# Performance work log

Measured on AMD Instinct MI355X. Metric: run time of the kernel, lower is better.

Reference implementation:

```python
import jax, jax.numpy as jnp
import numpy as np

EMBED_DIM = 1024
NUM_HEADS = 16
HEAD_DIM = EMBED_DIM // NUM_HEADS
SCALE = float(np.sqrt(HEAD_DIM))


def setup_inputs() -> dict:
    key = jax.random.key(0)
    ks = jax.random.split(key, 5)
    B, S, D = 4, 2048, EMBED_DIM
    lim_qkv = 1.0 / np.sqrt(D)
    lim_out = 1.0 / np.sqrt(D)
    return {
        "x": jax.random.normal(ks[0], (B, S, D), dtype=jnp.float32),
        "qkv_w": jax.random.uniform(ks[1], (3 * D, D), jnp.float32, -lim_qkv, lim_qkv),
        "qkv_b": jax.random.uniform(ks[2], (3 * D,), jnp.float32, -lim_qkv, lim_qkv),
        "out_w": jax.random.uniform(ks[3], (D, D), jnp.float32, -lim_out, lim_out),
        "out_b": jax.random.uniform(ks[4], (D,), jnp.float32, -lim_out, lim_out),
    }


def reference(x, qkv_w, qkv_b, out_w, out_b):
    B, S, D = x.shape
    H, Hd = NUM_HEADS, HEAD_DIM
    # qkv projection (torch Linear: x @ W.T + b)
    qkv = x @ qkv_w.T + qkv_b                      # [B, S, 3D]
    qkv = qkv.reshape(B, S, 3, H, Hd)
    q = jnp.transpose(qkv[:, :, 0], (0, 2, 1, 3))  # [B, H, S, Hd]
    k = jnp.transpose(qkv[:, :, 1], (0, 2, 1, 3))
    v = jnp.transpose(qkv[:, :, 2], (0, 2, 1, 3))
    attn = jnp.einsum("bhqd,bhkd->bhqk", q, k) / SCALE  # [B, H, S, S]
    attn = jax.nn.softmax(attn, axis=-1)
    out = jnp.einsum("bhqk,bhkd->bhqd", attn, v)        # [B, H, S, Hd]
    out = jnp.transpose(out, (0, 2, 1, 3)).reshape(B, S, D)
    return out @ out_w.T + out_b
```

## Files before the change

kernel.cpp:

```cpp
#include <hip/hip_runtime.h>

typedef unsigned short u16;
typedef __bf16 bf16x8 __attribute__((ext_vector_type(8)));
typedef __bf16 bf16x4 __attribute__((ext_vector_type(4)));
typedef float f32x4 __attribute__((ext_vector_type(4)));
typedef float f32x16 __attribute__((ext_vector_type(16)));
typedef unsigned u32x2 __attribute__((ext_vector_type(2)));

#define AS1 __attribute__((address_space(1)))
#define AS3 __attribute__((address_space(3)))

__device__ __forceinline__ void gload_lds16(const void* g, void* l) {
  __builtin_amdgcn_global_load_lds((const AS1 void*)g, (AS3 void*)l, 16, 0, 0);
}

__device__ __forceinline__ f32x4 mfma16(bf16x8 a, bf16x8 b, f32x4 c) {
  return __builtin_amdgcn_mfma_f32_16x16x32_bf16(a, b, c, 0, 0, 0);
}
__device__ __forceinline__ f32x16 mfma32(bf16x8 a, bf16x8 b, f32x16 c) {
  return __builtin_amdgcn_mfma_f32_32x32x16_bf16(a, b, c, 0, 0, 0);
}

#define QSCALE 0.18033688011112042f

__global__ __launch_bounds__(256) void k_cvt3(const float* __restrict__ s0, u16* __restrict__ d0, int n0,
                                              const float* __restrict__ s1, u16* __restrict__ d1, int n1,
                                              const float* __restrict__ s2, u16* __restrict__ d2, int n2) {
  int g = (blockIdx.x * 256 + threadIdx.x) * 8;
  const float* src;
  u16* dst;
  int i;
  if (g < n0) { src = s0; dst = d0; i = g; }
  else if (g < n0 + n1) { src = s1; dst = d1; i = g - n0; }
  else if (g < n0 + n1 + n2) { src = s2; dst = d2; i = g - n0 - n1; }
  else return;
  float4 a = *(const float4*)(src + i);
  float4 b = *(const float4*)(src + i + 4);
  union { bf16x8 v; uint4 q; } o;
  o.v[0] = (__bf16)a.x; o.v[1] = (__bf16)a.y; o.v[2] = (__bf16)a.z; o.v[3] = (__bf16)a.w;
  o.v[4] = (__bf16)b.x; o.v[5] = (__bf16)b.y; o.v[6] = (__bf16)b.z; o.v[7] = (__bf16)b.w;
  *(uint4*)(dst + i) = o.q;
}

template <int MODE>
__global__ __launch_bounds__(256) void k_gemm_bt(
    const u16* __restrict__ A, const u16* __restrict__ W,
    const float* __restrict__ bias, float* __restrict__ Cout,
    u16* __restrict__ Qo, u16* __restrict__ Ko, u16* __restrict__ Vo,
    int M, int N, int K) {
  __shared__ __align__(16) u16 As[128 * 64];
  __shared__ __align__(16) u16 Bs[128 * 64];
  const int t = threadIdx.x;
  const int m0 = blockIdx.y * 128;
  const int n0 = blockIdx.x * 128;
  const int lane = t & 63;
  const int w = t >> 6;
  const int lr = lane & 15;
  const int hi = lane >> 4;
  const int wm = (w >> 1) * 64;
  const int wn = (w & 1) * 64;

  f32x4 acc[4][4] = {};

  const u16* aptr = A + (size_t)(m0 + (t >> 3)) * K + (t & 7) * 8;
  const u16* wptr = W + (size_t)(n0 + (t >> 3)) * K + (t & 7) * 8;

  for (int kt = 0; kt < K; kt += 64) {
#pragma unroll
    for (int i = 0; i < 4; i++)
      gload_lds16(aptr + (size_t)i * 32 * K + kt, As + i * 2048 + t * 8);
#pragma unroll
    for (int i = 0; i < 4; i++)
      gload_lds16(wptr + (size_t)i * 32 * K + kt, Bs + i * 2048 + t * 8);
    __syncthreads();
#pragma unroll
    for (int kk = 0; kk < 64; kk += 32) {
      bf16x8 af[4], bfr[4];
#pragma unroll
      for (int mi = 0; mi < 4; mi++)
        af[mi] = *(const bf16x8*)(As + (wm + mi * 16 + lr) * 64 + kk + hi * 8);
#pragma unroll
      for (int ni = 0; ni < 4; ni++)
        bfr[ni] = *(const bf16x8*)(Bs + (wn + ni * 16 + lr) * 64 + kk + hi * 8);
#pragma unroll
      for (int mi = 0; mi < 4; mi++)
#pragma unroll
        for (int ni = 0; ni < 4; ni++)
          acc[mi][ni] = mfma16(af[mi], bfr[ni], acc[mi][ni]);
    }
    __syncthreads();
  }

  float bv[4];
#pragma unroll
  for (int ni = 0; ni < 4; ni++) bv[ni] = bias[n0 + wn + ni * 16 + lr];

  if (MODE == 0) {
#pragma unroll
    for (int mi = 0; mi < 4; mi++)
#pragma unroll
      for (int j = 0; j < 4; j++) {
        int m = m0 + wm + mi * 16 + hi * 4 + j;
#pragma unroll
        for (int ni = 0; ni < 4; ni++)
          Cout[(size_t)m * N + n0 + wn + ni * 16 + lr] = acc[mi][ni][j] + bv[ni];
      }
  } else {
    const int bb = m0 >> 11;
    const int sb0 = (m0 & 2047) + wm;
#pragma unroll
    for (int ni = 0; ni < 4; ni++) {
      int n = n0 + wn + ni * 16 + lr;
      int which = n >> 10;
      int h = (n >> 6) & 15;
      int hd = n & 63;
      if (which == 2) {
        u16* dst = Vo + ((size_t)((bb * 16 + h) * 64 + hd)) * 2048;
#pragma unroll
        for (int mi = 0; mi < 4; mi++) {
          int sb = sb0 + mi * 16 + hi * 4;
          bf16x4 pk;
#pragma unroll
          for (int j = 0; j < 4; j++) pk[j] = (__bf16)(acc[mi][ni][j] + bv[ni]);
          *(bf16x4*)(dst + sb) = pk;
        }
      } else {
        const float scl = (which == 0) ? QSCALE : 1.0f;
        u16* dst = ((which == 0) ? Qo : Ko) + (size_t)(bb * 16 + h) * 2048 * 64 + hd;
#pragma unroll
        for (int mi = 0; mi < 4; mi++)
#pragma unroll
          for (int j = 0; j < 4; j++) {
            int s = sb0 + mi * 16 + hi * 4 + j;
            union { __bf16 b; u16 u; } cv;
            cv.b = (__bf16)((acc[mi][ni][j] + bv[ni]) * scl);
            dst[(size_t)s * 64] = cv.u;
          }
      }
    }
  }
}

__global__ __launch_bounds__(256, 4) void k_attn(const u16* __restrict__ Q,
                                                 const u16* __restrict__ K,
                                                 const u16* __restrict__ Vt,
                                                 u16* __restrict__ ctx) {
  __shared__ __align__(16) u16 Ks[2][64 * 64];
  __shared__ __align__(16) u16 Vs[2][64 * 64];

  const int t = threadIdx.x;
  const int lane = t & 63;
  const int w = t >> 6;
  const int r31 = lane & 31;
  const int hw = lane >> 5;

  const int bid = blockIdx.x;
  const int nb = (bid & 7) * 128 + (bid >> 3);
  const int bh = nb >> 4;
  const int q0 = (nb & 15) * 128;

  const u16* qp = Q + (size_t)bh * 2048 * 64;
  const u16* kp = K + (size_t)bh * 2048 * 64;
  const u16* vp = Vt + (size_t)bh * 64 * 2048;

  const int tu = (t & 15) ^ (t >> 4);
  const int srow = (tu >> 3) * 32 + (t >> 4);
  const int scol = (tu & 7) * 8;

#pragma unroll
  for (int i = 0; i < 2; i++)
    gload_lds16(kp + (size_t)(srow + i * 16) * 64 + scol, Ks[0] + i * 2048 + t * 8);
#pragma unroll
  for (int i = 0; i < 2; i++)
    gload_lds16(vp + (size_t)(srow + i * 16) * 2048 + scol, Vs[0] + i * 2048 + t * 8);

  bf16x8 aq[4];
  const u16* qrow = qp + (size_t)(q0 + w * 32 + r31) * 64 + hw * 8;
#pragma unroll
  for (int kd = 0; kd < 4; kd++) aq[kd] = *(const bf16x8*)(qrow + kd * 16);

  bf16x8 ones;
#pragma unroll
  for (int e = 0; e < 8; e++) ones[e] = (__bf16)1.0f;

  asm volatile("s_waitcnt vmcnt(0)" ::: "memory");
  __builtin_amdgcn_sched_barrier(0);
  __builtin_amdgcn_s_barrier();
  __builtin_amdgcn_sched_barrier(0);

  f32x16 o0 = {}, o1 = {}, l_acc = {};

  for (int kt = 0; kt < 32; kt++) {
    const int cur = kt & 1;
    if (kt + 1 < 32) {
      u16* kd_ = Ks[cur ^ 1];
      u16* vd_ = Vs[cur ^ 1];
#pragma unroll
      for (int i = 0; i < 2; i++)
        gload_lds16(kp + (size_t)((kt + 1) * 64 + srow + i * 16) * 64 + scol,
                    kd_ + i * 2048 + t * 8);
#pragma unroll
      for (int i = 0; i < 2; i++)
        gload_lds16(vp + (size_t)(srow + i * 16) * 2048 + (kt + 1) * 64 + scol,
                    vd_ + i * 2048 + t * 8);
      asm volatile("s_waitcnt vmcnt(4)" ::: "memory");
    } else {
      asm volatile("s_waitcnt vmcnt(0)" ::: "memory");
    }
    __builtin_amdgcn_sched_barrier(0);
    __builtin_amdgcn_s_barrier();
    __builtin_amdgcn_sched_barrier(0);

    const u16* kb = Ks[cur];
    const u16* vb = Vs[cur];

    f32x16 s0 = {}, s1 = {};
    __builtin_amdgcn_s_setprio(1);
#pragma unroll
    for (int kd = 0; kd < 4; kd++) {
      int sl0 = (((kd * 2 + hw) ^ (r31 & 15)) << 3);
      int sl1 = (((8 + kd * 2 + hw) ^ (r31 & 15)) << 3);
      bf16x8 ka0 = *(const bf16x8*)(kb + r31 * 128 + sl0);
      bf16x8 ka1 = *(const bf16x8*)(kb + r31 * 128 + sl1);
      s0 = mfma32(ka0, aq[kd], s0);
      s1 = mfma32(ka1, aq[kd], s1);
    }
    __builtin_amdgcn_s_setprio(0);

#pragma unroll
    for (int e = 0; e < 16; e++) {
      s0[e] = __builtin_amdgcn_exp2f(s0[e]);
      s1[e] = __builtin_amdgcn_exp2f(s1[e]);
    }

    __builtin_amdgcn_s_setprio(1);
#pragma unroll
    for (int tile = 0; tile < 2; tile++) {
      f32x16 st = tile ? s1 : s0;
      unsigned pk[8];
#pragma unroll
      for (int p = 0; p < 8; p++) {
        union { __bf16 h[2]; unsigned u; } cv;
        cv.h[0] = (__bf16)st[2 * p];
        cv.h[1] = (__bf16)st[2 * p + 1];
        pk[p] = cv.u;
      }
#pragma unroll
      for (int c = 0; c < 2; c++) {
        u32x2 ra = __builtin_amdgcn_permlane32_swap(pk[4 * c], pk[4 * c + 2], false, false);
        u32x2 rb = __builtin_amdgcn_permlane32_swap(pk[4 * c + 1], pk[4 * c + 3], false, false);
        union { unsigned u[4]; bf16x8 v; } pf;
        pf.u[0] = ra[0]; pf.u[1] = rb[0]; pf.u[2] = ra[1]; pf.u[3] = rb[1];
        const int kap = tile * 2 + c;
        int slv0 = (((kap * 2 + hw) ^ (r31 & 15)) << 3);
        int slv1 = (((8 + kap * 2 + hw) ^ (r31 & 15)) << 3);
        bf16x8 v0 = *(const bf16x8*)(vb + r31 * 128 + slv0);
        bf16x8 v1 = *(const bf16x8*)(vb + r31 * 128 + slv1);
        o0 = mfma32(v0, pf.v, o0);
        o1 = mfma32(v1, pf.v, o1);
        l_acc = mfma32(ones, pf.v, l_acc);
      }
    }
    __builtin_amdgcn_s_setprio(0);
    __builtin_amdgcn_sched_barrier(0);
    __builtin_amdgcn_s_barrier();
  }

  const int bb = bh >> 4, h = bh & 15;
  const float inv = 1.0f / l_acc[0];
  const size_t base = (size_t)(bb * 2048 + q0 + w * 32 + r31) * 1024 + h * 64;
#pragma unroll
  for (int g = 0; g < 4; g++) {
    bf16x4 p0, p1;
#pragma unroll
    for (int j = 0; j < 4; j++) {
      p0[j] = (__bf16)(o0[g * 4 + j] * inv);
      p1[j] = (__bf16)(o1[g * 4 + j] * inv);
    }
    *(bf16x4*)(ctx + base + g * 8 + hw * 4) = p0;
    *(bf16x4*)(ctx + base + 32 + g * 8 + hw * 4) = p1;
  }
}

extern "C" void kernel_launch(void* const* d_in, const int* in_sizes, int n_in,
                              void* d_out, int out_size, void* d_ws, size_t ws_size,
                              hipStream_t stream) {
  const float* x = (const float*)d_in[0];
  const float* qkv_w = (const float*)d_in[1];
  const float* qkv_b = (const float*)d_in[2];
  const float* out_w = (const float*)d_in[3];
  const float* out_b = (const float*)d_in[4];
  float* out = (float*)d_out;
  char* ws = (char*)d_ws;

  u16* xb    = (u16*)(ws + 0);
  u16* wqkvb = (u16*)(ws + 16777216);
  u16* wob   = (u16*)(ws + 23068672);
  u16* Qb    = (u16*)(ws + 25165824);
  u16* Kb    = (u16*)(ws + 41943040);
  u16* Vtb   = (u16*)(ws + 58720256);
  u16* ctx   = xb;

  k_cvt3<<<6144, 256, 0, stream>>>(x, xb, 8388608,
                                   qkv_w, wqkvb, 3145728,
                                   out_w, wob, 1048576);

  k_gemm_bt<1><<<dim3(24, 64), 256, 0, stream>>>(xb, wqkvb, qkv_b, nullptr,
                                                 Qb, Kb, Vtb, 8192, 3072, 1024);
  k_attn<<<1024, 256, 0, stream>>>(Qb, Kb, Vtb, ctx);
  k_gemm_bt<0><<<dim3(8, 64), 256, 0, stream>>>(ctx, wob, out_b, out,
                                                nullptr, nullptr, nullptr,
                                                8192, 1024, 1024);
}
```

Baseline: 221.2 us.

## Rewrite QKV projection GEMM with larger tiles, double-buffered swizzled LDS and vectorized epilogue

Replaces the templated QKV GEMM with a dedicated 512-thread kernel that computes 256x128 tiles. It double-buffers the A and W tiles in LDS using XOR-swizzled direct global-to-LDS loads, remaps block IDs for L2 locality, and swaps MFMA operands so each lane holds contiguous head-dim values. Q and K are then written with vector bf16x4 stores instead of scalar strided stores, and V is transposed through LDS scratch so the transposed layout is written with 16-byte stores. The cost is higher LDS use (96 KB per block) and more register pressure, which limits occupancy to the declared two blocks per CU.

```diff
diff --git a/kernel.cpp b/kernel.cpp
--- a/kernel.cpp
+++ b/kernel.cpp
@@ -42,11 +42,138 @@
   *(uint4*)(dst + i) = o.q;
 }
 
-template <int MODE>
-__global__ __launch_bounds__(256) void k_gemm_bt(
+__global__ __launch_bounds__(512, 2) void k_gemm_qkv(
+    const u16* __restrict__ A, const u16* __restrict__ W,
+    const float* __restrict__ bias,
+    u16* __restrict__ Qo, u16* __restrict__ Ko, u16* __restrict__ Vo) {
+  __shared__ __align__(16) u16 LDS[2][6 * 4096];
+
+  const int t = threadIdx.x;
+  const int lane = t & 63;
+  const int w = t >> 6;
+  const int wm = w >> 1;
+  const int wn = w & 1;
+  const int lr = lane & 15;
+  const int hi = lane >> 4;
+
+  const int flat = blockIdx.x;
+  const int nb = (flat & 7) * 96 + (flat >> 3);
+  const int by = nb / 24;
+  const int bx = nb - by * 24;
+  const int m0 = by * 256;
+  const int n0 = bx * 128;
+
+  const int tt = t & 255;
+  const int g = t >> 8;
+  const int tu = (tt & 15) ^ (tt >> 4);
+  const int sro = (tu >> 3) * 32 + (tt >> 4);
+  const int scol = (tu & 7) * 8;
+
+  auto STAGE = [&](int buf, int kt) {
+#pragma unroll
+    for (int p = 0; p < 3; ++p) {
+      int st = p * 2 + g;
+      const u16* base = (st < 4) ? (A + (size_t)(m0 + st * 64) * 1024)
+                                 : (W + (size_t)(n0 + (st - 4) * 64) * 1024);
+#pragma unroll
+      for (int i = 0; i < 2; ++i)
+        gload_lds16(base + (size_t)(sro + i * 16) * 1024 + kt * 64 + scol,
+                    &LDS[buf][st * 4096 + i * 2048 + tt * 8]);
+    }
+  };
+
+  f32x4 acc[4][4] = {};
+
+  STAGE(0, 0);
+
+  for (int kt = 0; kt < 16; ++kt) {
+    const int cur = kt & 1;
+    asm volatile("s_waitcnt vmcnt(0)" ::: "memory");
+    __builtin_amdgcn_sched_barrier(0);
+    __builtin_amdgcn_s_barrier();
+    __builtin_amdgcn_sched_barrier(0);
+
+    if (kt + 1 < 16) STAGE(cur ^ 1, kt + 1);
+
+    const u16* ab = &LDS[cur][wm * 4096];
+    const u16* bb = &LDS[cur][(4 + wn) * 4096];
+
+    bf16x8 af[4][2], bfr[4][2];
+#pragma unroll
+    for (int mi = 0; mi < 4; ++mi)
+#pragma unroll
+      for (int ks = 0; ks < 2; ++ks)
+        af[mi][ks] = *(const bf16x8*)(ab + ((mi & 1) * 16 + lr) * 128 +
+                                      (((ks * 4 + hi + 8 * (mi >> 1)) ^ lr) << 3));
+#pragma unroll
+    for (int ni = 0; ni < 4; ++ni)
+#pragma unroll
+      for (int ks = 0; ks < 2; ++ks)
+        bfr[ni][ks] = *(const bf16x8*)(bb + ((ni & 1) * 16 + lr) * 128 +
+                                       (((ks * 4 + hi + 8 * (ni >> 1)) ^ lr) << 3));
+
+    __builtin_amdgcn_s_setprio(1);
+#pragma unroll
+    for (int mi = 0; mi < 4; ++mi)
+#pragma unroll
+      for (int ni = 0; ni < 4; ++ni)
+#pragma unroll
+        for (int ks = 0; ks < 2; ++ks)
+          acc[mi][ni] = mfma16(bfr[ni][ks], af[mi][ks], acc[mi][ni]);
+    __builtin_amdgcn_s_setprio(0);
+  }
+
+  const int bb16 = m0 >> 11;
+  const int sb = (m0 & 2047) + wm * 64;
+  const int which = n0 >> 10;
+  const int h = ((n0 & 1023) >> 6) + wn;
+  float4 bv[4];
+#pragma unroll
+  for (int ni = 0; ni < 4; ++ni)
+    bv[ni] = *(const float4*)(bias + n0 + wn * 64 + ni * 16 + hi * 4);
+
+  if (which < 2) {
+    const float scl = (which == 0) ? QSCALE : 1.0f;
+    u16* dst = ((which == 0) ? Qo : Ko) + ((size_t)(bb16 * 16 + h) * 2048) * 64;
+#pragma unroll
+    for (int mi = 0; mi < 4; ++mi) {
+      const int s = sb + mi * 16 + lr;
+#pragma unroll
+      for (int ni = 0; ni < 4; ++ni) {
+        bf16x4 pk;
+#pragma unroll
+        for (int j = 0; j < 4; ++j)
+          pk[j] = (__bf16)((acc[mi][ni][j] + ((const float*)&bv[ni])[j]) * scl);
+        *(bf16x4*)(dst + (size_t)s * 64 + ni * 16 + hi * 4) = pk;
+      }
+    }
+  } else {
+    __syncthreads();
+    u16* scr = &LDS[0][0] + w * 4608;
+#pragma unroll
+    for (int mi = 0; mi < 4; ++mi)
+#pragma unroll
+      for (int ni = 0; ni < 4; ++ni)
+#pragma unroll
+        for (int j = 0; j < 4; ++j) {
+          union { __bf16 b; u16 u; } cv;
+          cv.b = (__bf16)(acc[mi][ni][j] + ((const float*)&bv[ni])[j]);
+          scr[(ni * 16 + hi * 4 + j) * 72 + mi * 16 + lr] = cv.u;
+        }
+    asm volatile("s_waitcnt lgkmcnt(0)" ::: "memory");
+    __builtin_amdgcn_sched_barrier(0);
+    u16* dst = Vo + ((size_t)((bb16 * 16 + h) * 64 + lane)) * 2048 + sb;
+#pragma unroll
+    for (int mc = 0; mc < 8; ++mc) {
+      bf16x8 vv = *(const bf16x8*)(scr + lane * 72 + mc * 8);
+      *(bf16x8*)(dst + mc * 8) = vv;
+    }
+  }
+}
+
+__global__ __launch_bounds__(256) void k_gemm_out(
     const u16* __restrict__ A, const u16* __restrict__ W,
     const float* __restrict__ bias, float* __restrict__ Cout,
-    u16* __restrict__ Qo, u16* __restrict__ Ko, u16* __restrict__ Vo,
     int M, int N, int K) {
   __shared__ __align__(16) u16 As[128 * 64];
   __shared__ __align__(16) u16 Bs[128 * 64];
@@ -95,50 +222,15 @@
 #pragma unroll
   for (int ni = 0; ni < 4; ni++) bv[ni] = bias[n0 + wn + ni * 16 + lr];
 
-  if (MODE == 0) {
-#pragma unroll
-    for (int mi = 0; mi < 4; mi++)
-#pragma unroll
-      for (int j = 0; j < 4; j++) {
-        int m = m0 + wm + mi * 16 + hi * 4 + j;
-#pragma unroll
-        for (int ni = 0; ni < 4; ni++)
-          Cout[(size_t)m * N + n0 + wn + ni * 16 + lr] = acc[mi][ni][j] + bv[ni];
-      }
-  } else {
-    const int bb = m0 >> 11;
-    const int sb0 = (m0 & 2047) + wm;
-#pragma unroll
-    for (int ni = 0; ni < 4; ni++) {
-      int n = n0 + wn + ni * 16 + lr;
-      int which = n >> 10;
-      int h = (n >> 6) & 15;
-      int hd = n & 63;
-      if (which == 2) {
-        u16* dst = Vo + ((size_t)((bb * 16 + h) * 64 + hd)) * 2048;
-#pragma unroll
-        for (int mi = 0; mi < 4; mi++) {
-          int sb = sb0 + mi * 16 + hi * 4;
-          bf16x4 pk;
-#pragma unroll
-          for (int j = 0; j < 4; j++) pk[j] = (__bf16)(acc[mi][ni][j] + bv[ni]);
-          *(bf16x4*)(dst + sb) = pk;
-        }
-      } else {
-        const float scl = (which == 0) ? QSCALE : 1.0f;
-        u16* dst = ((which == 0) ? Qo : Ko) + (size_t)(bb * 16 + h) * 2048 * 64 + hd;
-#pragma unroll
-        for (int mi = 0; mi < 4; mi++)
-#pragma unroll
-          for (int j = 0; j < 4; j++) {
-            int s = sb0 + mi * 16 + hi * 4 + j;
-            union { __bf16 b; u16 u; } cv;
-            cv.b = (__bf16)((acc[mi][ni][j] + bv[ni]) * scl);
-            dst[(size_t)s * 64] = cv.u;
-          }
-      }
-    }
-  }
+#pragma unroll
+  for (int mi = 0; mi < 4; mi++)
+#pragma unroll
+    for (int j = 0; j < 4; j++) {
+      int m = m0 + wm + mi * 16 + hi * 4 + j;
+#pragma unroll
+      for (int ni = 0; ni < 4; ni++)
+        Cout[(size_t)m * N + n0 + wn + ni * 16 + lr] = acc[mi][ni][j] + bv[ni];
+    }
 }
 
 __global__ __launch_bounds__(256, 4) void k_attn(const u16* __restrict__ Q,
@@ -305,10 +397,8 @@
                                    qkv_w, wqkvb, 3145728,
                                    out_w, wob, 1048576);
 
-  k_gemm_bt<1><<<dim3(24, 64), 256, 0, stream>>>(xb, wqkvb, qkv_b, nullptr,
-                                                 Qb, Kb, Vtb, 8192, 3072, 1024);
+  k_gemm_qkv<<<768, 512, 0, stream>>>(xb, wqkvb, qkv_b, Qb, Kb, Vtb);
   k_attn<<<1024, 256, 0, stream>>>(Qb, Kb, Vtb, ctx);
-  k_gemm_bt<0><<<dim3(8, 64), 256, 0, stream>>>(ctx, wob, out_b, out,
-                                                nullptr, nullptr, nullptr,
-                                                8192, 1024, 1024);
-}
+  k_gemm_out<<<dim3(8, 64), 256, 0, stream>>>(ctx, wob, out_b, out,
+                                              8192, 1024, 1024);
+}
```

Measured after the change: 204.3 us. 7.7% less time.
